# Kernel optimization log

Measured on AMD Instinct MI355X. Metric: run time of the kernel, lower is better.

The kernel has to match this reference:

```python
import jax, jax.numpy as jnp
import numpy as np
from jax import lax

Z_DIM, X_DIM, Y_DIM, H_DIM = 128, 64, 64, 512


def setup_inputs() -> dict:
    key = jax.random.key(0)
    ks = jax.random.split(key, 10)
    s = 1.0 / np.sqrt(H_DIM)
    inp = {
        "z": jax.random.normal(ks[0], (1024, Z_DIM), dtype=jnp.float32),
        "x": jax.random.normal(ks[1], (1024, 32, X_DIM), dtype=jnp.float32),
        # LSTM params (PyTorch layout: gates ordered i,f,g,o)
        "W_ih": jax.random.uniform(ks[2], (4 * H_DIM, X_DIM), jnp.float32, -s, s),
        "W_hh": jax.random.uniform(ks[3], (4 * H_DIM, H_DIM), jnp.float32, -s, s),
        "b_ih": jax.random.uniform(ks[4], (4 * H_DIM,), jnp.float32, -s, s),
        "b_hh": jax.random.uniform(ks[5], (4 * H_DIM,), jnp.float32, -s, s),
        # proj_network: z_dim -> hidden
        "W_proj": jax.random.uniform(ks[6], (H_DIM, Z_DIM), jnp.float32, -s, s),
        "b_proj": jax.random.uniform(ks[7], (H_DIM,), jnp.float32, -s, s),
        # projout_network: hidden -> y_dim
        "W_out": jax.random.uniform(ks[8], (Y_DIM, H_DIM), jnp.float32, -s, s),
        "b_out": jax.random.uniform(ks[9], (Y_DIM,), jnp.float32, -s, s),
        "y_pred_len": 128,
    }
    return inp


def reference(z, x, W_ih, W_hh, b_ih, b_hh, W_proj, b_proj, W_out, b_out, y_pred_len):
    # initial recurrent state: h0 = c0 = proj(z)  [B, H]
    h0 = z @ W_proj.T + b_proj
    c0 = h0
    y_prev0 = x[:, -1, :]  # [B, X_DIM]

    def step(carry, _):
        h, c, y_prev = carry
        gates = y_prev @ W_ih.T + b_ih + h @ W_hh.T + b_hh  # [B, 4H]
        i, f, g, o = jnp.split(gates, 4, axis=-1)
        i = jax.nn.sigmoid(i)
        f = jax.nn.sigmoid(f)
        g = jnp.tanh(g)
        o = jax.nn.sigmoid(o)
        c = f * c + i * g
        h = o * jnp.tanh(c)
        y_cur = y_prev + (h @ W_out.T + b_out)  # residual (inference: feed back)
        return (h, c, y_cur), y_cur

    _, ys = lax.scan(step, (h0, c0, y_prev0), None, length=y_pred_len)
    return jnp.transpose(ys, (1, 0, 2))  # [B, T, Y_DIM]
```

## Files before the change

kernel.cpp:

```cpp
#include <hip/hip_runtime.h>
#include <stdint.h>

typedef _Float16 half8 __attribute__((ext_vector_type(8)));
typedef __attribute__((ext_vector_type(4))) float f4;
typedef __attribute__((ext_vector_type(4))) unsigned int u32x4;
typedef __attribute__((ext_vector_type(2))) unsigned int u32x2;

#define LDAH 200
#define EXS  34
#define HSTR 40

__device__ __forceinline__ float sigm(float x) { return 1.0f / (1.0f + __expf(-x)); }
__device__ __forceinline__ float tanh_(float x) { return 1.0f - 2.0f / (__expf(2.0f * x) + 1.0f); }


extern "C" __global__ void __launch_bounds__(256) k_wcat(
    const float* __restrict__ Wih, const float* __restrict__ Whh,
    _Float16* __restrict__ WA, _Float16* __restrict__ WB)
{
    int idx = blockIdx.x * 256 + threadIdx.x;
    int n = idx / 576, k = idx % 576;
    float v = (k < 64) ? Wih[n * 64 + k] : Whh[n * 512 + (k - 64)];
    _Float16 b = (_Float16)v;
    WA[idx] = b;
    if (k < 64) WB[idx] = b;
}

extern "C" __global__ void __launch_bounds__(256) k_comb(
    const float* __restrict__ Wih, const float* __restrict__ Whh,
    const float* __restrict__ Wo, _Float16* __restrict__ WB)
{
    int bx = blockIdx.x;
    int n = bx >> 1;
    int kh = ((bx & 1) << 8) + threadIdx.x;
    float acc = Whh[n * 512 + kh];
    #pragma unroll 16
    for (int p = 0; p < 64; ++p)
        acc += Wih[n * 64 + p] * Wo[p * 512 + kh];
    WB[n * 576 + 64 + kh] = (_Float16)acc;
}

extern "C" __global__ void __launch_bounds__(256) k_misc(
    const float* __restrict__ Wo, const float* __restrict__ bih, const float* __restrict__ bhh,
    const float* __restrict__ Wih, const float* __restrict__ bo, const float* __restrict__ x,
    _Float16* __restrict__ WoB, float* __restrict__ b0v, float* __restrict__ b1v,
    float* __restrict__ yf0, float* __restrict__ yf1,
    _Float16* __restrict__ yh0, _Float16* __restrict__ yh1,
    _Float16* __restrict__ yl0, _Float16* __restrict__ yl1)
{
    int idx = blockIdx.x * 256 + threadIdx.x;
    if (idx < 32768) { WoB[idx] = (_Float16)Wo[idx]; return; }
    if (idx < 34816) {
        int n = idx - 32768;
        float b = bih[n] + bhh[n];
        b0v[n] = b;
        float a = b;
        #pragma unroll 16
        for (int p = 0; p < 64; ++p) a += Wih[n * 64 + p] * bo[p];
        b1v[n] = a;
        return;
    }
    if (idx < 100352) {
        int e = idx - 34816;
        int m = e >> 6, nn = e & 63;
        float v = x[m * 2048 + 31 * 64 + nn];
        yf0[e] = v; yf1[e] = v;
        _Float16 hi = (_Float16)v;
        _Float16 lo = (_Float16)(v - (float)hi);
        yh0[e] = hi; yh1[e] = hi;
        yl0[e] = lo; yl1[e] = lo;
    }
}

extern "C" __global__ void __launch_bounds__(256) k_h0(
    const float* __restrict__ z, const float* __restrict__ Wp, const float* __restrict__ bp,
    float* __restrict__ cst, _Float16* __restrict__ hh0, _Float16* __restrict__ hl0)
{
    int bx = blockIdx.x;
    int m = bx >> 1;
    int n = ((bx & 1) << 8) + threadIdx.x;
    float acc = bp[n];
    const f4* zr = (const f4*)&z[m * 128];
    const f4* wr = (const f4*)&Wp[n * 128];
    #pragma unroll 8
    for (int p = 0; p < 32; ++p) {
        f4 zv = zr[p], wv = wr[p];
        acc += zv[0]*wv[0] + zv[1]*wv[1] + zv[2]*wv[2] + zv[3]*wv[3];
    }
    cst[m * 512 + n] = acc;
    _Float16 hi = (_Float16)acc;
    hh0[m * 512 + n] = hi;
    hl0[m * 512 + n] = (_Float16)(acc - (float)hi);
}

extern "C" __global__ void __launch_bounds__(256, 1) k_step(
    int t,
    const _Float16* __restrict__ Wcat,
    const float* __restrict__ bias,
    const _Float16* __restrict__ Wout,
    const float* __restrict__ bout,
    const _Float16* __restrict__ hh_in, const _Float16* __restrict__ hl_in,
    _Float16* __restrict__ hh_out, _Float16* __restrict__ hl_out,
    float* __restrict__ cst,
    const float* __restrict__ yf_in, float* __restrict__ yf_out,
    const _Float16* __restrict__ yh_in, _Float16* __restrict__ yh_out,
    const _Float16* __restrict__ yl_in, _Float16* __restrict__ yl_out,
    const float* __restrict__ dl_in, float* __restrict__ dl_out,
    float* __restrict__ out)
{
    __shared__ __align__(16) unsigned char smem[61440];
    _Float16* sAh = (_Float16*)smem;
    _Float16* sAl = (_Float16*)(smem + 25600);
    float*    sEx = (float*)smem;
    _Float16* sHh = (_Float16*)(smem + 51200);
    _Float16* sHl = (_Float16*)(smem + 56320);

    const int tid = threadIdx.x;
    const int bx  = blockIdx.x;
    const int mt  = bx >> 4, s = bx & 15;
    const int m0  = mt * 64, j0 = s * 32;

    if (t >= 1 && tid < 64) {
        int row = m0 + s * 4 + (tid >> 4);
        int c4  = (tid & 15) * 4;
        f4 a = *(const f4*)&yf_in[row * 64 + c4];
        a += *(const f4*)&bout[c4];
        #pragma unroll
        for (int sp = 0; sp < 16; ++sp)
            a += *(const f4*)&dl_in[sp * 65536 + row * 64 + c4];
        *(f4*)&yf_out[row * 64 + c4] = a;
        *(f4*)&out[row * 8192 + (t - 1) * 64 + c4] = a;
        _Float16 hi4[4], lo4[4];
        #pragma unroll
        for (int x = 0; x < 4; ++x) {
            hi4[x] = (_Float16)a[x];
            lo4[x] = (_Float16)(a[x] - (float)hi4[x]);
        }
        *(u32x2*)&yh_out[row * 64 + c4] = *(u32x2*)hi4;
        *(u32x2*)&yl_out[row * 64 + c4] = *(u32x2*)lo4;
    }
    if (t >= 128) return;

    const int wv = tid >> 6, lane = tid & 63, l15 = lane & 15, quad = lane >> 4;
    const int quad8 = quad * 8;

    f4 zero = {0.0f, 0.0f, 0.0f, 0.0f};
    f4 acc[4][2];
    #pragma unroll
    for (int a = 0; a < 4; ++a) { acc[a][0] = zero; acc[a][1] = zero; }

    const int brow0 = (wv * 512 + j0 + l15) * 576;
    const int brow1 = (wv * 512 + j0 + 16 + l15) * 576;

    int rr[6], cc6[6];
    #pragma unroll
    for (int it = 0; it < 6; ++it) {
        int i4 = it * 256 + tid;
        rr[it]  = i4 / 24;
        cc6[it] = (i4 % 24) * 8;
    }

    #pragma unroll
    for (int it = 0; it < 6; ++it) {
        int r = rr[it], cc = cc6[it];
        const _Float16 *sh, *sl;
        if (cc < 64) { sh = &yh_in[(m0 + r) * 64 + cc];        sl = &yl_in[(m0 + r) * 64 + cc]; }
        else         { sh = &hh_in[(m0 + r) * 512 + (cc - 64)]; sl = &hl_in[(m0 + r) * 512 + (cc - 64)]; }
        *(u32x4*)&sAh[r * LDAH + cc] = *(const u32x4*)sh;
        *(u32x4*)&sAl[r * LDAH + cc] = *(const u32x4*)sl;
    }

    u32x4 regH[6], regL[6];
    #pragma unroll
    for (int ch = 0; ch < 3; ++ch) {
        half8 bv0[6], bv1[6];
        #pragma unroll
        for (int kc = 0; kc < 6; ++kc) {
            int bq = ch * 192 + kc * 32 + quad8;
            bv0[kc] = *(const half8*)&Wcat[brow0 + bq];
            bv1[kc] = *(const half8*)&Wcat[brow1 + bq];
        }
        if (ch < 2) {
            #pragma unroll
            for (int it = 0; it < 6; ++it) {
                int c = (ch + 1) * 192 + cc6[it] - 64;
                regH[it] = *(const u32x4*)&hh_in[(m0 + rr[it]) * 512 + c];
                regL[it] = *(const u32x4*)&hl_in[(m0 + rr[it]) * 512 + c];
            }
        }
        __syncthreads();
        #pragma unroll
        for (int kc = 0; kc < 6; ++kc) {
            int kq = kc * 32 + quad8;
            half8 ah0 = *(const half8*)&sAh[(l15     ) * LDAH + kq];
            half8 ah1 = *(const half8*)&sAh[(l15 + 16) * LDAH + kq];
            half8 ah2 = *(const half8*)&sAh[(l15 + 32) * LDAH + kq];
            half8 ah3 = *(const half8*)&sAh[(l15 + 48) * LDAH + kq];
            half8 al0 = *(const half8*)&sAl[(l15     ) * LDAH + kq];
            half8 al1 = *(const half8*)&sAl[(l15 + 16) * LDAH + kq];
            half8 al2 = *(const half8*)&sAl[(l15 + 32) * LDAH + kq];
            half8 al3 = *(const half8*)&sAl[(l15 + 48) * LDAH + kq];
            acc[0][0] = __builtin_amdgcn_mfma_f32_16x16x32_f16(ah0, bv0[kc], acc[0][0], 0, 0, 0);
            acc[1][0] = __builtin_amdgcn_mfma_f32_16x16x32_f16(ah1, bv0[kc], acc[1][0], 0, 0, 0);
            acc[2][0] = __builtin_amdgcn_mfma_f32_16x16x32_f16(ah2, bv0[kc], acc[2][0], 0, 0, 0);
            acc[3][0] = __builtin_amdgcn_mfma_f32_16x16x32_f16(ah3, bv0[kc], acc[3][0], 0, 0, 0);
            acc[0][1] = __builtin_amdgcn_mfma_f32_16x16x32_f16(ah0, bv1[kc], acc[0][1], 0, 0, 0);
            acc[1][1] = __builtin_amdgcn_mfma_f32_16x16x32_f16(ah1, bv1[kc], acc[1][1], 0, 0, 0);
            acc[2][1] = __builtin_amdgcn_mfma_f32_16x16x32_f16(ah2, bv1[kc], acc[2][1], 0, 0, 0);
            acc[3][1] = __builtin_amdgcn_mfma_f32_16x16x32_f16(ah3, bv1[kc], acc[3][1], 0, 0, 0);
            acc[0][0] = __builtin_amdgcn_mfma_f32_16x16x32_f16(al0, bv0[kc], acc[0][0], 0, 0, 0);
            acc[1][0] = __builtin_amdgcn_mfma_f32_16x16x32_f16(al1, bv0[kc], acc[1][0], 0, 0, 0);
            acc[2][0] = __builtin_amdgcn_mfma_f32_16x16x32_f16(al2, bv0[kc], acc[2][0], 0, 0, 0);
            acc[3][0] = __builtin_amdgcn_mfma_f32_16x16x32_f16(al3, bv0[kc], acc[3][0], 0, 0, 0);
            acc[0][1] = __builtin_amdgcn_mfma_f32_16x16x32_f16(al0, bv1[kc], acc[0][1], 0, 0, 0);
            acc[1][1] = __builtin_amdgcn_mfma_f32_16x16x32_f16(al1, bv1[kc], acc[1][1], 0, 0, 0);
            acc[2][1] = __builtin_amdgcn_mfma_f32_16x16x32_f16(al2, bv1[kc], acc[2][1], 0, 0, 0);
            acc[3][1] = __builtin_amdgcn_mfma_f32_16x16x32_f16(al3, bv1[kc], acc[3][1], 0, 0, 0);
        }
        if (ch < 2) {
            __syncthreads();
            #pragma unroll
            for (int it = 0; it < 6; ++it) {
                *(u32x4*)&sAh[rr[it] * LDAH + cc6[it]] = regH[it];
                *(u32x4*)&sAl[rr[it] * LDAH + cc6[it]] = regL[it];
            }
        }
    }
    __syncthreads();

    #pragma unroll
    for (int a = 0; a < 4; ++a)
        #pragma unroll
        for (int b = 0; b < 2; ++b)
            #pragma unroll
            for (int r = 0; r < 4; ++r)
                sEx[(wv * 64 + a * 16 + quad * 4 + r) * EXS + b * 16 + l15] = acc[a][b][r];
    __syncthreads();

    {
        int m = tid >> 2, jb = (tid & 3) * 8;
        int jcol = j0 + jb;
        int crow = (m0 + m) * 512 + jcol;
        f4 c0 = *(const f4*)&cst[crow];
        f4 c1 = *(const f4*)&cst[crow + 4];
        _Float16 hi8[8], lo8[8];
        #pragma unroll
        for (int x = 0; x < 8; ++x) {
            float gi = sEx[(0 * 64 + m) * EXS + jb + x] + bias[       jcol + x];
            float gf = sEx[(1 * 64 + m) * EXS + jb + x] + bias[ 512 + jcol + x];
            float gg = sEx[(2 * 64 + m) * EXS + jb + x] + bias[1024 + jcol + x];
            float go = sEx[(3 * 64 + m) * EXS + jb + x] + bias[1536 + jcol + x];
            float iv = sigm(gi), fv = sigm(gf), gv = tanh_(gg), ov = sigm(go);
            float cold = (x < 4) ? c0[x] : c1[x - 4];
            float cn = fv * cold + iv * gv;
            float hn = ov * tanh_(cn);
            if (x < 4) c0[x] = cn; else c1[x - 4] = cn;
            _Float16 hi = (_Float16)hn;
            hi8[x] = hi;
            lo8[x] = (_Float16)(hn - (float)hi);
        }
        *(f4*)&cst[crow]     = c0;
        *(f4*)&cst[crow + 4] = c1;
        *(u32x4*)&hh_out[crow]       = *(u32x4*)hi8;
        *(u32x4*)&hl_out[crow]       = *(u32x4*)lo8;
        *(u32x4*)&sHh[m * HSTR + jb] = *(u32x4*)hi8;
        *(u32x4*)&sHl[m * HSTR + jb] = *(u32x4*)lo8;
    }
    __syncthreads();

    {
        half8 bw = *(const half8*)&Wout[(wv * 16 + l15) * 512 + j0 + quad8];
        f4 d[4];
        #pragma unroll
        for (int a = 0; a < 4; ++a) d[a] = zero;
        #pragma unroll
        for (int a = 0; a < 4; ++a) {
            half8 ahh = *(const half8*)&sHh[(a * 16 + l15) * HSTR + quad8];
            half8 ahl = *(const half8*)&sHl[(a * 16 + l15) * HSTR + quad8];
            d[a] = __builtin_amdgcn_mfma_f32_16x16x32_f16(ahh, bw, d[a], 0, 0, 0);
            d[a] = __builtin_amdgcn_mfma_f32_16x16x32_f16(ahl, bw, d[a], 0, 0, 0);
        }
        #pragma unroll
        for (int a = 0; a < 4; ++a)
            #pragma unroll
            for (int r = 0; r < 4; ++r)
                dl_out[s * 65536 + (m0 + a * 16 + quad * 4 + r) * 64 + wv * 16 + l15] = d[a][r];
    }
}

extern "C" void kernel_launch(void* const* d_in, const int* in_sizes, int n_in,
                              void* d_out, int out_size, void* d_ws, size_t ws_size,
                              hipStream_t stream)
{
    const float* z   = (const float*)d_in[0];
    const float* x   = (const float*)d_in[1];
    const float* Wih = (const float*)d_in[2];
    const float* Whh = (const float*)d_in[3];
    const float* bih = (const float*)d_in[4];
    const float* bhh = (const float*)d_in[5];
    const float* Wp  = (const float*)d_in[6];
    const float* bp  = (const float*)d_in[7];
    const float* Wo  = (const float*)d_in[8];
    const float* bo  = (const float*)d_in[9];

    char* w = (char*)d_ws;
    _Float16* WA  = (_Float16*)w; w += 2359296;
    _Float16* WB  = (_Float16*)w; w += 2359296;
    _Float16* WoB = (_Float16*)w; w += 65536;
    float* b0v = (float*)w; w += 8192;
    float* b1v = (float*)w; w += 8192;
    _Float16* hh[2];
    hh[0] = (_Float16*)w; w += 1048576;
    hh[1] = (_Float16*)w; w += 1048576;
    _Float16* hl[2];
    hl[0] = (_Float16*)w; w += 1048576;
    hl[1] = (_Float16*)w; w += 1048576;
    float* cst = (float*)w; w += 2097152;
    float* yf[2];
    yf[0] = (float*)w; w += 262144;
    yf[1] = (float*)w; w += 262144;
    _Float16* yh[2];
    yh[0] = (_Float16*)w; w += 131072;
    yh[1] = (_Float16*)w; w += 131072;
    _Float16* yl[2];
    yl[0] = (_Float16*)w; w += 131072;
    yl[1] = (_Float16*)w; w += 131072;
    float* dl[2];
    dl[0] = (float*)w; w += 4194304;
    dl[1] = (float*)w; w += 4194304;
    float* out = (float*)d_out;

    k_wcat<<<4608, 256, 0, stream>>>(Wih, Whh, WA, WB);
    k_comb<<<4096, 256, 0, stream>>>(Wih, Whh, Wo, WB);
    k_misc<<<392, 256, 0, stream>>>(Wo, bih, bhh, Wih, bo, x, WoB, b0v, b1v,
                                    yf[0], yf[1], yh[0], yh[1], yl[0], yl[1]);
    k_h0<<<2048, 256, 0, stream>>>(z, Wp, bp, cst, hh[0], hl[0]);

    for (int t = 0; t <= 128; ++t) {
        k_step<<<256, 256, 0, stream>>>(t,
            (t == 0) ? WA : WB, (t == 0) ? b0v : b1v,
            WoB, bo,
            hh[t & 1], hl[t & 1], hh[(t + 1) & 1], hl[(t + 1) & 1],
            cst,
            yf[t & 1], yf[(t + 1) & 1],
            yh[t & 1], yh[(t + 1) & 1],
            yl[t & 1], yl[(t + 1) & 1],
            dl[(t + 1) & 1], dl[t & 1],
            out);
    }
}
```

Measured before the change: 1.997 ms.

## Split step kernel over 512 threads and defer y resolve to kernel tail

Each step block now runs 8 waves instead of 4, so each wave computes one 16-column gate tile instead of two. This halves per-wave accumulators and weight registers, and the weight chunks are double-buffered across K chunks. The y residual reduction moves from the kernel head to the tail (or runs alone at the final step), so it no longer delays the GEMM start. The cell update is spread over twice as many threads with biases and the cell state preloaded early. Risks include more barriers across 8 waves, a different register budget under launch_bounds(512,2), and the LDS exchange stride changing to 36.

```diff
diff --git a/kernel.cpp b/kernel.cpp
--- a/kernel.cpp
+++ b/kernel.cpp
@@ -7,7 +7,7 @@
 typedef __attribute__((ext_vector_type(2))) unsigned int u32x2;
 
 #define LDAH 200
-#define EXS  34
+#define EXS  36
 #define HSTR 40
 
 __device__ __forceinline__ float sigm(float x) { return 1.0f / (1.0f + __expf(-x)); }
@@ -93,7 +93,32 @@
     hl0[m * 512 + n] = (_Float16)(acc - (float)hi);
 }
 
-extern "C" __global__ void __launch_bounds__(256, 1) k_step(
+
+__device__ __forceinline__ void resolve_y(
+    int t, int row, int c4,
+    const float* __restrict__ yf_in, float* __restrict__ yf_out,
+    const float* __restrict__ dl_in, const float* __restrict__ bout,
+    _Float16* __restrict__ yh_out, _Float16* __restrict__ yl_out,
+    float* __restrict__ out)
+{
+    f4 a = *(const f4*)&yf_in[row * 64 + c4];
+    a += *(const f4*)&bout[c4];
+    #pragma unroll
+    for (int sp = 0; sp < 16; ++sp)
+        a += *(const f4*)&dl_in[sp * 65536 + row * 64 + c4];
+    *(f4*)&yf_out[row * 64 + c4] = a;
+    *(f4*)&out[row * 8192 + (t - 1) * 64 + c4] = a;
+    _Float16 hi4[4], lo4[4];
+    #pragma unroll
+    for (int x = 0; x < 4; ++x) {
+        hi4[x] = (_Float16)a[x];
+        lo4[x] = (_Float16)(a[x] - (float)hi4[x]);
+    }
+    *(u32x2*)&yh_out[row * 64 + c4] = *(u32x2*)hi4;
+    *(u32x2*)&yl_out[row * 64 + c4] = *(u32x2*)lo4;
+}
+
+extern "C" __global__ void __launch_bounds__(512, 2) k_step(
     int t,
     const _Float16* __restrict__ Wcat,
     const float* __restrict__ bias,
@@ -120,171 +145,159 @@
     const int mt  = bx >> 4, s = bx & 15;
     const int m0  = mt * 64, j0 = s * 32;
 
+    if (t >= 128) {
+        if (tid < 64) {
+            int row = m0 + s * 4 + (tid >> 4);
+            int c4  = (tid & 15) * 4;
+            resolve_y(t, row, c4, yf_in, yf_out, dl_in, bout, yh_out, yl_out, out);
+        }
+        return;
+    }
+
+    const int w = tid >> 6, lane = tid & 63, l15 = lane & 15, quad = lane >> 4;
+    const int quad8 = quad * 8;
+    const int q = w >> 1, hx = w & 1;
+
+    const int cm = tid >> 3, cjb = (tid & 7) * 4;
+    const int cjcol = j0 + cjb;
+    const int ccrow = (m0 + cm) * 512 + cjcol;
+    f4 cpre = *(const f4*)&cst[ccrow];
+    f4 bi0 = *(const f4*)&bias[       cjcol];
+    f4 bi1 = *(const f4*)&bias[ 512 + cjcol];
+    f4 bi2 = *(const f4*)&bias[1024 + cjcol];
+    f4 bi3 = *(const f4*)&bias[1536 + cjcol];
+    const int dn = w >> 1, ap = w & 1;
+    half8 bw = *(const half8*)&Wout[(dn * 16 + l15) * 512 + j0 + quad8];
+
+    const int brow = (q * 512 + j0 + hx * 16 + l15) * 576;
+
+    half8 bv[2][6];
+    #pragma unroll
+    for (int kc = 0; kc < 6; ++kc)
+        bv[0][kc] = *(const half8*)&Wcat[brow + kc * 32 + quad8];
+
+    int rr[3], cc3[3];
+    #pragma unroll
+    for (int it = 0; it < 3; ++it) {
+        int i4 = it * 512 + tid;
+        rr[it]  = i4 / 24;
+        cc3[it] = (i4 % 24) * 8;
+    }
+
+    #pragma unroll
+    for (int it = 0; it < 3; ++it) {
+        int r = rr[it], cc = cc3[it];
+        const _Float16 *sh, *sl;
+        if (cc < 64) { sh = &yh_in[(m0 + r) * 64 + cc];         sl = &yl_in[(m0 + r) * 64 + cc]; }
+        else         { sh = &hh_in[(m0 + r) * 512 + (cc - 64)]; sl = &hl_in[(m0 + r) * 512 + (cc - 64)]; }
+        *(u32x4*)&sAh[r * LDAH + cc] = *(const u32x4*)sh;
+        *(u32x4*)&sAl[r * LDAH + cc] = *(const u32x4*)sl;
+    }
+
+    f4 zero = {0.0f, 0.0f, 0.0f, 0.0f};
+    f4 acc[4];
+    acc[0] = zero; acc[1] = zero; acc[2] = zero; acc[3] = zero;
+
+    u32x4 regH[3], regL[3];
+    #pragma unroll
+    for (int ch = 0; ch < 3; ++ch) {
+        if (ch < 2) {
+            #pragma unroll
+            for (int it = 0; it < 3; ++it) {
+                int c = (ch + 1) * 192 + cc3[it] - 64;
+                regH[it] = *(const u32x4*)&hh_in[(m0 + rr[it]) * 512 + c];
+                regL[it] = *(const u32x4*)&hl_in[(m0 + rr[it]) * 512 + c];
+            }
+            #pragma unroll
+            for (int kc = 0; kc < 6; ++kc)
+                bv[(ch + 1) & 1][kc] = *(const half8*)&Wcat[brow + (ch + 1) * 192 + kc * 32 + quad8];
+        }
+        __syncthreads();
+        #pragma unroll
+        for (int kc = 0; kc < 6; ++kc) {
+            int kq = kc * 32 + quad8;
+            half8 b = bv[ch & 1][kc];
+            #pragma unroll
+            for (int a = 0; a < 4; ++a) {
+                half8 ah = *(const half8*)&sAh[(l15 + a * 16) * LDAH + kq];
+                acc[a] = __builtin_amdgcn_mfma_f32_16x16x32_f16(ah, b, acc[a], 0, 0, 0);
+            }
+            #pragma unroll
+            for (int a = 0; a < 4; ++a) {
+                half8 al = *(const half8*)&sAl[(l15 + a * 16) * LDAH + kq];
+                acc[a] = __builtin_amdgcn_mfma_f32_16x16x32_f16(al, b, acc[a], 0, 0, 0);
+            }
+        }
+        if (ch < 2) {
+            __syncthreads();
+            #pragma unroll
+            for (int it = 0; it < 3; ++it) {
+                *(u32x4*)&sAh[rr[it] * LDAH + cc3[it]] = regH[it];
+                *(u32x4*)&sAl[rr[it] * LDAH + cc3[it]] = regL[it];
+            }
+        }
+    }
+    __syncthreads();
+
+    #pragma unroll
+    for (int a = 0; a < 4; ++a)
+        #pragma unroll
+        for (int r = 0; r < 4; ++r)
+            sEx[(q * 64 + a * 16 + quad * 4 + r) * EXS + hx * 16 + l15] = acc[a][r];
+    __syncthreads();
+
+    {
+        f4 c0 = cpre;
+        f4 gI = *(const f4*)&sEx[(0 * 64 + cm) * EXS + cjb];
+        f4 gF = *(const f4*)&sEx[(1 * 64 + cm) * EXS + cjb];
+        f4 gG = *(const f4*)&sEx[(2 * 64 + cm) * EXS + cjb];
+        f4 gO = *(const f4*)&sEx[(3 * 64 + cm) * EXS + cjb];
+        _Float16 hi4[4], lo4[4];
+        #pragma unroll
+        for (int x = 0; x < 4; ++x) {
+            float iv = sigm(gI[x] + bi0[x]);
+            float fv = sigm(gF[x] + bi1[x]);
+            float gv = tanh_(gG[x] + bi2[x]);
+            float ov = sigm(gO[x] + bi3[x]);
+            float cn = fv * c0[x] + iv * gv;
+            float hn = ov * tanh_(cn);
+            c0[x] = cn;
+            _Float16 hi = (_Float16)hn;
+            hi4[x] = hi;
+            lo4[x] = (_Float16)(hn - (float)hi);
+        }
+        *(f4*)&cst[ccrow] = c0;
+        *(u32x2*)&hh_out[ccrow]        = *(u32x2*)hi4;
+        *(u32x2*)&hl_out[ccrow]        = *(u32x2*)lo4;
+        *(u32x2*)&sHh[cm * HSTR + cjb] = *(u32x2*)hi4;
+        *(u32x2*)&sHl[cm * HSTR + cjb] = *(u32x2*)lo4;
+    }
+    __syncthreads();
+
+    {
+        f4 d[2];
+        d[0] = zero; d[1] = zero;
+        #pragma unroll
+        for (int a2 = 0; a2 < 2; ++a2) {
+            int a = ap * 2 + a2;
+            half8 ahh = *(const half8*)&sHh[(a * 16 + l15) * HSTR + quad8];
+            half8 ahl = *(const half8*)&sHl[(a * 16 + l15) * HSTR + quad8];
+            d[a2] = __builtin_amdgcn_mfma_f32_16x16x32_f16(ahh, bw, d[a2], 0, 0, 0);
+            d[a2] = __builtin_amdgcn_mfma_f32_16x16x32_f16(ahl, bw, d[a2], 0, 0, 0);
+        }
+        #pragma unroll
+        for (int a2 = 0; a2 < 2; ++a2) {
+            int a = ap * 2 + a2;
+            #pragma unroll
+            for (int r = 0; r < 4; ++r)
+                dl_out[s * 65536 + (m0 + a * 16 + quad * 4 + r) * 64 + dn * 16 + l15] = d[a2][r];
+        }
+    }
+
     if (t >= 1 && tid < 64) {
         int row = m0 + s * 4 + (tid >> 4);
         int c4  = (tid & 15) * 4;
-        f4 a = *(const f4*)&yf_in[row * 64 + c4];
-        a += *(const f4*)&bout[c4];
-        #pragma unroll
-        for (int sp = 0; sp < 16; ++sp)
-            a += *(const f4*)&dl_in[sp * 65536 + row * 64 + c4];
-        *(f4*)&yf_out[row * 64 + c4] = a;
-        *(f4*)&out[row * 8192 + (t - 1) * 64 + c4] = a;
-        _Float16 hi4[4], lo4[4];
-        #pragma unroll
-        for (int x = 0; x < 4; ++x) {
-            hi4[x] = (_Float16)a[x];
-            lo4[x] = (_Float16)(a[x] - (float)hi4[x]);
-        }
-        *(u32x2*)&yh_out[row * 64 + c4] = *(u32x2*)hi4;
-        *(u32x2*)&yl_out[row * 64 + c4] = *(u32x2*)lo4;
-    }
-    if (t >= 128) return;
-
-    const int wv = tid >> 6, lane = tid & 63, l15 = lane & 15, quad = lane >> 4;
-    const int quad8 = quad * 8;
-
-    f4 zero = {0.0f, 0.0f, 0.0f, 0.0f};
-    f4 acc[4][2];
-    #pragma unroll
-    for (int a = 0; a < 4; ++a) { acc[a][0] = zero; acc[a][1] = zero; }
-
-    const int brow0 = (wv * 512 + j0 + l15) * 576;
-    const int brow1 = (wv * 512 + j0 + 16 + l15) * 576;
-
-    int rr[6], cc6[6];
-    #pragma unroll
-    for (int it = 0; it < 6; ++it) {
-        int i4 = it * 256 + tid;
-        rr[it]  = i4 / 24;
-        cc6[it] = (i4 % 24) * 8;
-    }
-
-    #pragma unroll
-    for (int it = 0; it < 6; ++it) {
-        int r = rr[it], cc = cc6[it];
-        const _Float16 *sh, *sl;
-        if (cc < 64) { sh = &yh_in[(m0 + r) * 64 + cc];        sl = &yl_in[(m0 + r) * 64 + cc]; }
-        else         { sh = &hh_in[(m0 + r) * 512 + (cc - 64)]; sl = &hl_in[(m0 + r) * 512 + (cc - 64)]; }
-        *(u32x4*)&sAh[r * LDAH + cc] = *(const u32x4*)sh;
-        *(u32x4*)&sAl[r * LDAH + cc] = *(const u32x4*)sl;
-    }
-
-    u32x4 regH[6], regL[6];
-    #pragma unroll
-    for (int ch = 0; ch < 3; ++ch) {
-        half8 bv0[6], bv1[6];
-        #pragma unroll
-        for (int kc = 0; kc < 6; ++kc) {
-            int bq = ch * 192 + kc * 32 + quad8;
-            bv0[kc] = *(const half8*)&Wcat[brow0 + bq];
-            bv1[kc] = *(const half8*)&Wcat[brow1 + bq];
-        }
-        if (ch < 2) {
-            #pragma unroll
-            for (int it = 0; it < 6; ++it) {
-                int c = (ch + 1) * 192 + cc6[it] - 64;
-                regH[it] = *(const u32x4*)&hh_in[(m0 + rr[it]) * 512 + c];
-                regL[it] = *(const u32x4*)&hl_in[(m0 + rr[it]) * 512 + c];
-            }
-        }
-        __syncthreads();
-        #pragma unroll
-        for (int kc = 0; kc < 6; ++kc) {
-            int kq = kc * 32 + quad8;
-            half8 ah0 = *(const half8*)&sAh[(l15     ) * LDAH + kq];
-            half8 ah1 = *(const half8*)&sAh[(l15 + 16) * LDAH + kq];
-            half8 ah2 = *(const half8*)&sAh[(l15 + 32) * LDAH + kq];
-            half8 ah3 = *(const half8*)&sAh[(l15 + 48) * LDAH + kq];
-            half8 al0 = *(const half8*)&sAl[(l15     ) * LDAH + kq];
-            half8 al1 = *(const half8*)&sAl[(l15 + 16) * LDAH + kq];
-            half8 al2 = *(const half8*)&sAl[(l15 + 32) * LDAH + kq];
-            half8 al3 = *(const half8*)&sAl[(l15 + 48) * LDAH + kq];
-            acc[0][0] = __builtin_amdgcn_mfma_f32_16x16x32_f16(ah0, bv0[kc], acc[0][0], 0, 0, 0);
-            acc[1][0] = __builtin_amdgcn_mfma_f32_16x16x32_f16(ah1, bv0[kc], acc[1][0], 0, 0, 0);
-            acc[2][0] = __builtin_amdgcn_mfma_f32_16x16x32_f16(ah2, bv0[kc], acc[2][0], 0, 0, 0);
-            acc[3][0] = __builtin_amdgcn_mfma_f32_16x16x32_f16(ah3, bv0[kc], acc[3][0], 0, 0, 0);
-            acc[0][1] = __builtin_amdgcn_mfma_f32_16x16x32_f16(ah0, bv1[kc], acc[0][1], 0, 0, 0);
-            acc[1][1] = __builtin_amdgcn_mfma_f32_16x16x32_f16(ah1, bv1[kc], acc[1][1], 0, 0, 0);
-            acc[2][1] = __builtin_amdgcn_mfma_f32_16x16x32_f16(ah2, bv1[kc], acc[2][1], 0, 0, 0);
-            acc[3][1] = __builtin_amdgcn_mfma_f32_16x16x32_f16(ah3, bv1[kc], acc[3][1], 0, 0, 0);
-            acc[0][0] = __builtin_amdgcn_mfma_f32_16x16x32_f16(al0, bv0[kc], acc[0][0], 0, 0, 0);
-            acc[1][0] = __builtin_amdgcn_mfma_f32_16x16x32_f16(al1, bv0[kc], acc[1][0], 0, 0, 0);
-            acc[2][0] = __builtin_amdgcn_mfma_f32_16x16x32_f16(al2, bv0[kc], acc[2][0], 0, 0, 0);
-            acc[3][0] = __builtin_amdgcn_mfma_f32_16x16x32_f16(al3, bv0[kc], acc[3][0], 0, 0, 0);
-            acc[0][1] = __builtin_amdgcn_mfma_f32_16x16x32_f16(al0, bv1[kc], acc[0][1], 0, 0, 0);
-            acc[1][1] = __builtin_amdgcn_mfma_f32_16x16x32_f16(al1, bv1[kc], acc[1][1], 0, 0, 0);
-            acc[2][1] = __builtin_amdgcn_mfma_f32_16x16x32_f16(al2, bv1[kc], acc[2][1], 0, 0, 0);
-            acc[3][1] = __builtin_amdgcn_mfma_f32_16x16x32_f16(al3, bv1[kc], acc[3][1], 0, 0, 0);
-        }
-        if (ch < 2) {
-            __syncthreads();
-            #pragma unroll
-            for (int it = 0; it < 6; ++it) {
-                *(u32x4*)&sAh[rr[it] * LDAH + cc6[it]] = regH[it];
-                *(u32x4*)&sAl[rr[it] * LDAH + cc6[it]] = regL[it];
-            }
-        }
-    }
-    __syncthreads();
-
-    #pragma unroll
-    for (int a = 0; a < 4; ++a)
-        #pragma unroll
-        for (int b = 0; b < 2; ++b)
-            #pragma unroll
-            for (int r = 0; r < 4; ++r)
-                sEx[(wv * 64 + a * 16 + quad * 4 + r) * EXS + b * 16 + l15] = acc[a][b][r];
-    __syncthreads();
-
-    {
-        int m = tid >> 2, jb = (tid & 3) * 8;
-        int jcol = j0 + jb;
-        int crow = (m0 + m) * 512 + jcol;
-        f4 c0 = *(const f4*)&cst[crow];
-        f4 c1 = *(const f4*)&cst[crow + 4];
-        _Float16 hi8[8], lo8[8];
-        #pragma unroll
-        for (int x = 0; x < 8; ++x) {
-            float gi = sEx[(0 * 64 + m) * EXS + jb + x] + bias[       jcol + x];
-            float gf = sEx[(1 * 64 + m) * EXS + jb + x] + bias[ 512 + jcol + x];
-            float gg = sEx[(2 * 64 + m) * EXS + jb + x] + bias[1024 + jcol + x];
-            float go = sEx[(3 * 64 + m) * EXS + jb + x] + bias[1536 + jcol + x];
-            float iv = sigm(gi), fv = sigm(gf), gv = tanh_(gg), ov = sigm(go);
-            float cold = (x < 4) ? c0[x] : c1[x - 4];
-            float cn = fv * cold + iv * gv;
-            float hn = ov * tanh_(cn);
-            if (x < 4) c0[x] = cn; else c1[x - 4] = cn;
-            _Float16 hi = (_Float16)hn;
-            hi8[x] = hi;
-            lo8[x] = (_Float16)(hn - (float)hi);
-        }
-        *(f4*)&cst[crow]     = c0;
-        *(f4*)&cst[crow + 4] = c1;
-        *(u32x4*)&hh_out[crow]       = *(u32x4*)hi8;
-        *(u32x4*)&hl_out[crow]       = *(u32x4*)lo8;
-        *(u32x4*)&sHh[m * HSTR + jb] = *(u32x4*)hi8;
-        *(u32x4*)&sHl[m * HSTR + jb] = *(u32x4*)lo8;
-    }
-    __syncthreads();
-
-    {
-        half8 bw = *(const half8*)&Wout[(wv * 16 + l15) * 512 + j0 + quad8];
-        f4 d[4];
-        #pragma unroll
-        for (int a = 0; a < 4; ++a) d[a] = zero;
-        #pragma unroll
-        for (int a = 0; a < 4; ++a) {
-            half8 ahh = *(const half8*)&sHh[(a * 16 + l15) * HSTR + quad8];
-            half8 ahl = *(const half8*)&sHl[(a * 16 + l15) * HSTR + quad8];
-            d[a] = __builtin_amdgcn_mfma_f32_16x16x32_f16(ahh, bw, d[a], 0, 0, 0);
-            d[a] = __builtin_amdgcn_mfma_f32_16x16x32_f16(ahl, bw, d[a], 0, 0, 0);
-        }
-        #pragma unroll
-        for (int a = 0; a < 4; ++a)
-            #pragma unroll
-            for (int r = 0; r < 4; ++r)
-                dl_out[s * 65536 + (m0 + a * 16 + quad * 4 + r) * 64 + wv * 16 + l15] = d[a][r];
+        resolve_y(t, row, c4, yf_in, yf_out, dl_in, bout, yh_out, yl_out, out);
     }
 }
 
@@ -337,7 +350,7 @@
     k_h0<<<2048, 256, 0, stream>>>(z, Wp, bp, cst, hh[0], hl[0]);
 
     for (int t = 0; t <= 128; ++t) {
-        k_step<<<256, 256, 0, stream>>>(t,
+        k_step<<<256, 512, 0, stream>>>(t,
             (t == 0) ? WA : WB, (t == 0) ? b0v : b1v,
             WoB, bo,
             hh[t & 1], hl[t & 1], hh[(t + 1) & 1], hl[(t + 1) & 1],
```

Result: slower. 2.183 ms (+9.3%).

## Double-buffer A tiles in LDS and prefetch weight fragments one chunk ahead

Applied to the files above, without the earlier changes.

The A-operand tiles in shared memory are now double-buffered, so the next K-chunk is written into the alternate buffer and each chunk needs one barrier instead of two. Weight fragments are register-prefetched one chunk ahead, with the first chunk loaded before the initial A staging. Shared memory grows to about 110 KB and register pressure rises from the doubled B fragments. The point is to hide global load latency behind the MFMA work.

```diff
diff --git a/kernel.cpp b/kernel.cpp
--- a/kernel.cpp
+++ b/kernel.cpp
@@ -108,12 +108,16 @@
     const float* __restrict__ dl_in, float* __restrict__ dl_out,
     float* __restrict__ out)
 {
-    __shared__ __align__(16) unsigned char smem[61440];
-    _Float16* sAh = (_Float16*)smem;
-    _Float16* sAl = (_Float16*)(smem + 25600);
-    float*    sEx = (float*)smem;
-    _Float16* sHh = (_Float16*)(smem + 51200);
-    _Float16* sHl = (_Float16*)(smem + 56320);
+    __shared__ __align__(16) unsigned char smem[112640];
+    _Float16* sAh0 = (_Float16*)smem;
+    _Float16* sAl0 = (_Float16*)(smem + 25600);
+    _Float16* sAh1 = (_Float16*)(smem + 51200);
+    _Float16* sAl1 = (_Float16*)(smem + 76800);
+    float*    sEx  = (float*)smem;
+    _Float16* sHh  = (_Float16*)(smem + 102400);
+    _Float16* sHl  = (_Float16*)(smem + 107520);
+    _Float16* const sAh[2] = { sAh0, sAh1 };
+    _Float16* const sAl[2] = { sAl0, sAl1 };
 
     const int tid = threadIdx.x;
     const int bx  = blockIdx.x;
@@ -152,6 +156,13 @@
     const int brow0 = (wv * 512 + j0 + l15) * 576;
     const int brow1 = (wv * 512 + j0 + 16 + l15) * 576;
 
+    half8 bv0[2][6], bv1[2][6];
+    #pragma unroll
+    for (int kc = 0; kc < 6; ++kc) {
+        bv0[0][kc] = *(const half8*)&Wcat[brow0 + kc * 32 + quad8];
+        bv1[0][kc] = *(const half8*)&Wcat[brow1 + kc * 32 + quad8];
+    }
+
     int rr[6], cc6[6];
     #pragma unroll
     for (int it = 0; it < 6; ++it) {
@@ -164,22 +175,16 @@
     for (int it = 0; it < 6; ++it) {
         int r = rr[it], cc = cc6[it];
         const _Float16 *sh, *sl;
-        if (cc < 64) { sh = &yh_in[(m0 + r) * 64 + cc];        sl = &yl_in[(m0 + r) * 64 + cc]; }
+        if (cc < 64) { sh = &yh_in[(m0 + r) * 64 + cc];         sl = &yl_in[(m0 + r) * 64 + cc]; }
         else         { sh = &hh_in[(m0 + r) * 512 + (cc - 64)]; sl = &hl_in[(m0 + r) * 512 + (cc - 64)]; }
-        *(u32x4*)&sAh[r * LDAH + cc] = *(const u32x4*)sh;
-        *(u32x4*)&sAl[r * LDAH + cc] = *(const u32x4*)sl;
-    }
+        *(u32x4*)&sAh0[r * LDAH + cc] = *(const u32x4*)sh;
+        *(u32x4*)&sAl0[r * LDAH + cc] = *(const u32x4*)sl;
+    }
+    __syncthreads();
 
     u32x4 regH[6], regL[6];
     #pragma unroll
     for (int ch = 0; ch < 3; ++ch) {
-        half8 bv0[6], bv1[6];
-        #pragma unroll
-        for (int kc = 0; kc < 6; ++kc) {
-            int bq = ch * 192 + kc * 32 + quad8;
-            bv0[kc] = *(const half8*)&Wcat[brow0 + bq];
-            bv1[kc] = *(const half8*)&Wcat[brow1 + bq];
-        }
         if (ch < 2) {
             #pragma unroll
             for (int it = 0; it < 6; ++it) {
@@ -187,43 +192,52 @@
                 regH[it] = *(const u32x4*)&hh_in[(m0 + rr[it]) * 512 + c];
                 regL[it] = *(const u32x4*)&hl_in[(m0 + rr[it]) * 512 + c];
             }
-        }
-        __syncthreads();
+            #pragma unroll
+            for (int kc = 0; kc < 6; ++kc) {
+                bv0[(ch + 1) & 1][kc] = *(const half8*)&Wcat[brow0 + (ch + 1) * 192 + kc * 32 + quad8];
+                bv1[(ch + 1) & 1][kc] = *(const half8*)&Wcat[brow1 + (ch + 1) * 192 + kc * 32 + quad8];
+            }
+        }
+        const _Float16* Ah = sAh[ch & 1];
+        const _Float16* Al = sAl[ch & 1];
         #pragma unroll
         for (int kc = 0; kc < 6; ++kc) {
             int kq = kc * 32 + quad8;
-            half8 ah0 = *(const half8*)&sAh[(l15     ) * LDAH + kq];
-            half8 ah1 = *(const half8*)&sAh[(l15 + 16) * LDAH + kq];
-            half8 ah2 = *(const half8*)&sAh[(l15 + 32) * LDAH + kq];
-            half8 ah3 = *(const half8*)&sAh[(l15 + 48) * LDAH + kq];
-            half8 al0 = *(const half8*)&sAl[(l15     ) * LDAH + kq];
-            half8 al1 = *(const half8*)&sAl[(l15 + 16) * LDAH + kq];
-            half8 al2 = *(const half8*)&sAl[(l15 + 32) * LDAH + kq];
-            half8 al3 = *(const half8*)&sAl[(l15 + 48) * LDAH + kq];
-            acc[0][0] = __builtin_amdgcn_mfma_f32_16x16x32_f16(ah0, bv0[kc], acc[0][0], 0, 0, 0);
-            acc[1][0] = __builtin_amdgcn_mfma_f32_16x16x32_f16(ah1, bv0[kc], acc[1][0], 0, 0, 0);
-            acc[2][0] = __builtin_amdgcn_mfma_f32_16x16x32_f16(ah2, bv0[kc], acc[2][0], 0, 0, 0);
-            acc[3][0] = __builtin_amdgcn_mfma_f32_16x16x32_f16(ah3, bv0[kc], acc[3][0], 0, 0, 0);
-            acc[0][1] = __builtin_amdgcn_mfma_f32_16x16x32_f16(ah0, bv1[kc], acc[0][1], 0, 0, 0);
-            acc[1][1] = __builtin_amdgcn_mfma_f32_16x16x32_f16(ah1, bv1[kc], acc[1][1], 0, 0, 0);
-            acc[2][1] = __builtin_amdgcn_mfma_f32_16x16x32_f16(ah2, bv1[kc], acc[2][1], 0, 0, 0);
-            acc[3][1] = __builtin_amdgcn_mfma_f32_16x16x32_f16(ah3, bv1[kc], acc[3][1], 0, 0, 0);
-            acc[0][0] = __builtin_amdgcn_mfma_f32_16x16x32_f16(al0, bv0[kc], acc[0][0], 0, 0, 0);
-            acc[1][0] = __builtin_amdgcn_mfma_f32_16x16x32_f16(al1, bv0[kc], acc[1][0], 0, 0, 0);
-            acc[2][0] = __builtin_amdgcn_mfma_f32_16x16x32_f16(al2, bv0[kc], acc[2][0], 0, 0, 0);
-            acc[3][0] = __builtin_amdgcn_mfma_f32_16x16x32_f16(al3, bv0[kc], acc[3][0], 0, 0, 0);
-            acc[0][1] = __builtin_amdgcn_mfma_f32_16x16x32_f16(al0, bv1[kc], acc[0][1], 0, 0, 0);
-            acc[1][1] = __builtin_amdgcn_mfma_f32_16x16x32_f16(al1, bv1[kc], acc[1][1], 0, 0, 0);
-            acc[2][1] = __builtin_amdgcn_mfma_f32_16x16x32_f16(al2, bv1[kc], acc[2][1], 0, 0, 0);
-            acc[3][1] = __builtin_amdgcn_mfma_f32_16x16x32_f16(al3, bv1[kc], acc[3][1], 0, 0, 0);
+            half8 b0 = bv0[ch & 1][kc], b1 = bv1[ch & 1][kc];
+            half8 ah0 = *(const half8*)&Ah[(l15     ) * LDAH + kq];
+            half8 ah1 = *(const half8*)&Ah[(l15 + 16) * LDAH + kq];
+            half8 ah2 = *(const half8*)&Ah[(l15 + 32) * LDAH + kq];
+            half8 ah3 = *(const half8*)&Ah[(l15 + 48) * LDAH + kq];
+            acc[0][0] = __builtin_amdgcn_mfma_f32_16x16x32_f16(ah0, b0, acc[0][0], 0, 0, 0);
+            acc[1][0] = __builtin_amdgcn_mfma_f32_16x16x32_f16(ah1, b0, acc[1][0], 0, 0, 0);
+            acc[2][0] = __builtin_amdgcn_mfma_f32_16x16x32_f16(ah2, b0, acc[2][0], 0, 0, 0);
+            acc[3][0] = __builtin_amdgcn_mfma_f32_16x16x32_f16(ah3, b0, acc[3][0], 0, 0, 0);
+            acc[0][1] = __builtin_amdgcn_mfma_f32_16x16x32_f16(ah0, b1, acc[0][1], 0, 0, 0);
+            acc[1][1] = __builtin_amdgcn_mfma_f32_16x16x32_f16(ah1, b1, acc[1][1], 0, 0, 0);
+            acc[2][1] = __builtin_amdgcn_mfma_f32_16x16x32_f16(ah2, b1, acc[2][1], 0, 0, 0);
+            acc[3][1] = __builtin_amdgcn_mfma_f32_16x16x32_f16(ah3, b1, acc[3][1], 0, 0, 0);
+            half8 al0 = *(const half8*)&Al[(l15     ) * LDAH + kq];
+            half8 al1 = *(const half8*)&Al[(l15 + 16) * LDAH + kq];
+            half8 al2 = *(const half8*)&Al[(l15 + 32) * LDAH + kq];
+            half8 al3 = *(const half8*)&Al[(l15 + 48) * LDAH + kq];
+            acc[0][0] = __builtin_amdgcn_mfma_f32_16x16x32_f16(al0, b0, acc[0][0], 0, 0, 0);
+            acc[1][0] = __builtin_amdgcn_mfma_f32_16x16x32_f16(al1, b0, acc[1][0], 0, 0, 0);
+            acc[2][0] = __builtin_amdgcn_mfma_f32_16x16x32_f16(al2, b0, acc[2][0], 0, 0, 0);
+            acc[3][0] = __builtin_amdgcn_mfma_f32_16x16x32_f16(al3, b0, acc[3][0], 0, 0, 0);
+            acc[0][1] = __builtin_amdgcn_mfma_f32_16x16x32_f16(al0, b1, acc[0][1], 0, 0, 0);
+            acc[1][1] = __builtin_amdgcn_mfma_f32_16x16x32_f16(al1, b1, acc[1][1], 0, 0, 0);
+            acc[2][1] = __builtin_amdgcn_mfma_f32_16x16x32_f16(al2, b1, acc[2][1], 0, 0, 0);
+            acc[3][1] = __builtin_amdgcn_mfma_f32_16x16x32_f16(al3, b1, acc[3][1], 0, 0, 0);
         }
         if (ch < 2) {
+            _Float16* Dh = sAh[(ch + 1) & 1];
+            _Float16* Dl = sAl[(ch + 1) & 1];
+            #pragma unroll
+            for (int it = 0; it < 6; ++it) {
+                *(u32x4*)&Dh[rr[it] * LDAH + cc6[it]] = regH[it];
+                *(u32x4*)&Dl[rr[it] * LDAH + cc6[it]] = regL[it];
+            }
             __syncthreads();
-            #pragma unroll
-            for (int it = 0; it < 6; ++it) {
-                *(u32x4*)&sAh[rr[it] * LDAH + cc6[it]] = regH[it];
-                *(u32x4*)&sAl[rr[it] * LDAH + cc6[it]] = regL[it];
-            }
         }
     }
     __syncthreads();
```

Result: no change. 2.012 ms (+0.7%).
